# Kernel optimization log

Hardware: AMD Instinct MI355X
Metric: run time of the kernel (lower is better)

## Reference

```python
import jax, jax.numpy as jnp
import numpy as np

B, C, E_OLD, U = 8, 128, 48000, 8000
E_NEW = E_OLD + 3 * U  # unroll_target = 72000


def setup_inputs() -> dict:
    key = jax.random.key(0)
    kf, kw, kp = jax.random.split(key, 3)
    features = jax.random.normal(kf, (B, C, E_OLD), dtype=jnp.float32)
    weights = jax.random.uniform(kw, (B, U, 2, 3), dtype=jnp.float32)
    # Per-mesh permutation of the unrolled edge slots -> disjoint index groups
    perms = jax.vmap(lambda k: jax.random.permutation(k, E_NEW))(
        jax.random.split(kp, B)
    ).astype(jnp.int32)
    old_idx = perms[:, :E_OLD]                      # slots of relocated old edges
    left_idx = old_idx[:, :U]                       # source edges of unpool events
    right_idx = old_idx[:, U:2 * U]
    new_block = perms[:, E_OLD:]                    # 3U brand-new slots
    new_idx = new_block[:, :U]
    new_left_idx = new_block[:, U:2 * U]
    new_right_idx = new_block[:, 2 * U:3 * U]
    return {
        "features": features,
        "weights": weights,
        "old_idx": old_idx,
        "left_idx": left_idx,
        "right_idx": right_idx,
        "new_idx": new_idx,
        "new_left_idx": new_left_idx,
        "new_right_idx": new_right_idx,
    }


def _unpool_one(feat, w, old_i, l_i, r_i, n_i, nl_i, nr_i):
    # feat: [C, E_OLD], w: [U, 2, 3]
    nf = jnp.zeros((feat.shape[0], E_NEW), feat.dtype).at[:, old_i].set(feat)
    lf = nf[:, l_i]                                 # [C, U] left source features
    rf = nf[:, r_i]                                 # [C, U]
    lw, rw = w[:, 0, :], w[:, 1, :]                 # [U, 3] each
    nf = nf.at[:, l_i].set(lf * lw[:, 0])
    nf = nf.at[:, nl_i].set(lf * lw[:, 1])
    nf = nf.at[:, r_i].set(rf * rw[:, 0])
    nf = nf.at[:, nr_i].set(rf * rw[:, 1])
    nf = nf.at[:, n_i].set((lf * lw[:, 2] + rf * rw[:, 2]) * 0.5)
    return nf


def reference(features, weights, old_idx, left_idx, right_idx, new_idx,
              new_left_idx, new_right_idx):
    return jax.vmap(_unpool_one)(features, weights, old_idx, left_idx,
                                 right_idx, new_idx, new_left_idx,
                                 new_right_idx)  # [B, C, E_NEW]
```

## Files before the change

kernel.cpp:

```cpp
#include <hip/hip_runtime.h>


constexpr int B_     = 8;
constexpr int C_     = 128;
constexpr int E_OLD_ = 48000;
constexpr int U_     = 8000;
constexpr int E_NEW_ = E_OLD_ + 3 * U_;
constexpr int T_PER_B = U_ + (E_OLD_ - 2 * U_);

__device__ __forceinline__ int4 pack_map(int s0, int s1, float w0, float w1) {
    return make_int4(s0, s1, __float_as_int(w0), __float_as_int(w1));
}

__global__ __launch_bounds__(256)
void build_map_kernel(const float* __restrict__ w,
                      const int*   __restrict__ old_idx,
                      const int*   __restrict__ new_idx,
                      const int*   __restrict__ new_left,
                      const int*   __restrict__ new_right,
                      int4*        __restrict__ map) {
    const int b = blockIdx.y;
    const int t = blockIdx.x * blockDim.x + threadIdx.x;
    if (t >= T_PER_B) return;

    int4* mb = map + (size_t)b * E_NEW_;

    if (t < U_) {
        const int u   = t;
        const int jl  = old_idx [b * E_OLD_ + u];
        const int jr  = old_idx [b * E_OLD_ + U_ + u];
        const int jn  = new_idx [b * U_ + u];
        const int jnl = new_left [b * U_ + u];
        const int jnr = new_right[b * U_ + u];

        const float* wp = w + ((size_t)b * U_ + u) * 6;
        const float lw0 = wp[0], lw1 = wp[1], lw2 = wp[2];
        const float rw0 = wp[3], rw1 = wp[4], rw2 = wp[5];

        mb[jl]  = pack_map(u,       u,       lw0,        0.f);
        mb[jnl] = pack_map(u,       u,       lw1,        0.f);
        mb[jr]  = pack_map(U_ + u,  U_ + u,  rw0,        0.f);
        mb[jnr] = pack_map(U_ + u,  U_ + u,  rw1,        0.f);
        mb[jn]  = pack_map(u,       U_ + u,  0.5f * lw2, 0.5f * rw2);
    } else {
        const int e = t + U_;
        const int j = old_idx[b * E_OLD_ + e];
        mb[j] = pack_map(e, e, 1.0f, 0.f);
    }
}

constexpr int TE = 128;
constexpr int TC = 64;

__global__ __launch_bounds__(256)
void transpose_kernel(const float* __restrict__ feat,
                      float*       __restrict__ featT,
                      int b0) {
    __shared__ float tile[TE][TC + 1];
    const int bl = blockIdx.z;
    const int b  = b0 + bl;
    const int e0 = blockIdx.x * TE;
    const int c0 = blockIdx.y * TC;
    const int t  = threadIdx.x;

    {
        const int eo = (t & 31) * 4;
        const int co = t >> 5;
        const float* fb = feat + (size_t)b * C_ * E_OLD_ + e0 + eo;
        #pragma unroll
        for (int i = 0; i < 8; ++i) {
            const int c = i * 8 + co;
            const float4 v = *(const float4*)(fb + (size_t)(c0 + c) * E_OLD_);
            tile[eo + 0][c] = v.x;
            tile[eo + 1][c] = v.y;
            tile[eo + 2][c] = v.z;
            tile[eo + 3][c] = v.w;
        }
    }
    __syncthreads();

    {
        const int c4 = (t & 15) * 4;
        const int eb = t >> 4;
        float* ft = featT + (size_t)bl * E_OLD_ * C_
                          + (size_t)e0 * C_ + c0 + c4;
        #pragma unroll
        for (int i = 0; i < 8; ++i) {
            const int e = i * 16 + eb;
            float4 v;
            v.x = tile[e][c4 + 0];
            v.y = tile[e][c4 + 1];
            v.z = tile[e][c4 + 2];
            v.w = tile[e][c4 + 3];
            *(float4*)(ft + (size_t)e * C_) = v;
        }
    }
}

constexpr int JT = 64;
constexpr int TILES_PER_B = E_NEW_ / JT;

__global__ __launch_bounds__(256)
void gatherT_kernel(const float* __restrict__ featT,
                    const int4*  __restrict__ map,
                    float*       __restrict__ out,
                    int b0, int nb) {
    __shared__ float tile[JT][133];
    const int bl    = blockIdx.x % nb;
    const int b     = b0 + bl;
    const int chunk = blockIdx.x / nb;
    const int j0    = chunk * JT;
    const int t     = threadIdx.x;

    {
        const int j  = t >> 2;
        const int cq = t & 3;
        const int4 m = map[(size_t)b * E_NEW_ + j0 + j];
        const float w0 = __int_as_float(m.z);
        const float w1 = __int_as_float(m.w);

        const float* fTb = featT + (size_t)bl * E_OLD_ * C_;
        const float4* r0 = (const float4*)(fTb + (size_t)m.x * C_) + cq * 8;

        float4 acc[8];
        #pragma unroll
        for (int i = 0; i < 8; ++i) {
            const float4 f = r0[i];
            acc[i].x = w0 * f.x;
            acc[i].y = w0 * f.y;
            acc[i].z = w0 * f.z;
            acc[i].w = w0 * f.w;
        }
        if (w1 != 0.f) {
            const float4* r1 = (const float4*)(fTb + (size_t)m.y * C_) + cq * 8;
            #pragma unroll
            for (int i = 0; i < 8; ++i) {
                const float4 f = r1[i];
                acc[i].x += w1 * f.x;
                acc[i].y += w1 * f.y;
                acc[i].z += w1 * f.z;
                acc[i].w += w1 * f.w;
            }
        }
        float* trow = &tile[j][cq * 32];
        #pragma unroll
        for (int i = 0; i < 8; ++i) {
            trow[4 * i + 0] = acc[i].x;
            trow[4 * i + 1] = acc[i].y;
            trow[4 * i + 2] = acc[i].z;
            trow[4 * i + 3] = acc[i].w;
        }
    }
    __syncthreads();

    {
        const int jj = t & 63;
        const int cg = t >> 6;
        const float* tr = &tile[jj][cg * 32];
        float* ob = out + (size_t)b * C_ * E_NEW_
                        + (size_t)(cg * 32) * E_NEW_ + j0 + jj;
        #pragma unroll
        for (int k = 0; k < 32; ++k)
            __builtin_nontemporal_store(tr[k], ob + (size_t)k * E_NEW_);
    }
}

constexpr int K2_BLOCK     = 256;
constexpr int CHUNKS_PER_B = (E_NEW_ + K2_BLOCK - 1) / K2_BLOCK;

__global__ __launch_bounds__(K2_BLOCK)
void gather_kernel(const float* __restrict__ feat,
                   const int4*  __restrict__ map,
                   float*       __restrict__ out) {
    const int b     = blockIdx.x % B_;
    const int chunk = blockIdx.x / B_;
    const int j     = chunk * K2_BLOCK + threadIdx.x;
    if (j >= E_NEW_) return;

    const int4 m  = map[(size_t)b * E_NEW_ + j];
    const int  s0 = m.x;
    const int  s1 = m.y;
    const float w0 = __int_as_float(m.z);
    const float w1 = __int_as_float(m.w);

    const float* fb = feat + (size_t)b * C_ * E_OLD_;
    float*       ob = out  + (size_t)b * C_ * E_NEW_ + j;

    #pragma unroll 4
    for (int c = 0; c < C_; ++c) {
        const float f0 = fb[s0];
        const float f1 = fb[s1];
        *ob = w0 * f0 + w1 * f1;
        fb += E_OLD_;
        ob += E_NEW_;
    }
}

extern "C" void kernel_launch(void* const* d_in, const int* in_sizes, int n_in,
                              void* d_out, int out_size, void* d_ws, size_t ws_size,
                              hipStream_t stream) {
    const float* feat      = (const float*)d_in[0];
    const float* w         = (const float*)d_in[1];
    const int*   old_idx   = (const int*)  d_in[2];
    const int*   new_idx   = (const int*)  d_in[5];
    const int*   new_left  = (const int*)  d_in[6];
    const int*   new_right = (const int*)  d_in[7];
    float*       out       = (float*)d_out;

    int4* map = (int4*)d_ws;
    const size_t map_bytes = (size_t)B_ * E_NEW_ * sizeof(int4);
    const size_t featT_off = (map_bytes + 255) & ~(size_t)255;
    const size_t featT_one = (size_t)E_OLD_ * C_ * sizeof(float);
    const size_t featT_all = (size_t)B_ * featT_one;
    float* featT = (float*)((char*)d_ws + featT_off);

    {
        dim3 block(256);
        dim3 grid((T_PER_B + 255) / 256, B_);
        build_map_kernel<<<grid, block, 0, stream>>>(
            w, old_idx, new_idx, new_left, new_right, map);
    }

    if (ws_size >= featT_off + featT_all) {
        {
            dim3 block(256);
            dim3 grid(E_OLD_ / TE, C_ / TC, B_);
            transpose_kernel<<<grid, block, 0, stream>>>(feat, featT, 0);
        }
        {
            dim3 block(256);
            dim3 grid(TILES_PER_B * B_);
            gatherT_kernel<<<grid, block, 0, stream>>>(featT, map, out, 0, B_);
        }
    } else if (ws_size >= featT_off + featT_one) {
        for (int b = 0; b < B_; ++b) {
            dim3 tblock(256);
            dim3 tgrid(E_OLD_ / TE, C_ / TC, 1);
            transpose_kernel<<<tgrid, tblock, 0, stream>>>(feat, featT, b);
            dim3 gblock(256);
            dim3 ggrid(TILES_PER_B);
            gatherT_kernel<<<ggrid, gblock, 0, stream>>>(featT, map, out, b, 1);
        }
    } else {
        dim3 block(K2_BLOCK);
        dim3 grid(CHUNKS_PER_B * B_);
        gather_kernel<<<grid, block, 0, stream>>>(feat, map, out);
    }
}
```

Before: 558.8 us.

## Software-pipeline per-batch transpose and gather in fused step kernels

Replaces the separate build-map, all-batch transpose and all-batch gather launches with a sequence of combined step kernels. Step k transposes batch k and gathers batch k-1 in the same grid, and step 0 also builds the index map. The aim is to overlap transpose reads with gather writes and to keep each batch's transposed features hot in cache until they are gathered. In exchange it adds more launches, a pipeline tail, and blocks that exit early with no work. The device-side bodies are factored into shared inline helpers, and the fallback paths are preserved.

```diff
diff --git a/kernel.cpp b/kernel.cpp
--- a/kernel.cpp
+++ b/kernel.cpp
@@ -8,8 +8,187 @@
 constexpr int E_NEW_ = E_OLD_ + 3 * U_;
 constexpr int T_PER_B = U_ + (E_OLD_ - 2 * U_);
 
+constexpr int TE = 128;
+constexpr int TC = 64;
+constexpr int JT = 64;
+
+constexpr int T_BLOCKS    = (E_OLD_ / TE) * (C_ / TC);
+constexpr int G_BLOCKS    = E_NEW_ / JT;
+constexpr int BM_BLOCKS   = (B_ * T_PER_B + 255) / 256;
+
+constexpr int LDS_WORDS = 64 * 133;
+
 __device__ __forceinline__ int4 pack_map(int s0, int s1, float w0, float w1) {
     return make_int4(s0, s1, __float_as_int(w0), __float_as_int(w1));
+}
+
+
+__device__ __forceinline__ void build_body(
+    const float* __restrict__ w,
+    const int*   __restrict__ old_idx,
+    const int*   __restrict__ new_idx,
+    const int*   __restrict__ new_left,
+    const int*   __restrict__ new_right,
+    int4*        __restrict__ map,
+    int b, int t) {
+    int4* mb = map + (size_t)b * E_NEW_;
+
+    if (t < U_) {
+        const int u   = t;
+        const int jl  = old_idx [b * E_OLD_ + u];
+        const int jr  = old_idx [b * E_OLD_ + U_ + u];
+        const int jn  = new_idx [b * U_ + u];
+        const int jnl = new_left [b * U_ + u];
+        const int jnr = new_right[b * U_ + u];
+
+        const float* wp = w + ((size_t)b * U_ + u) * 6;
+        const float lw0 = wp[0], lw1 = wp[1], lw2 = wp[2];
+        const float rw0 = wp[3], rw1 = wp[4], rw2 = wp[5];
+
+        mb[jl]  = pack_map(u,       u,       lw0,        0.f);
+        mb[jnl] = pack_map(u,       u,       lw1,        0.f);
+        mb[jr]  = pack_map(U_ + u,  U_ + u,  rw0,        0.f);
+        mb[jnr] = pack_map(U_ + u,  U_ + u,  rw1,        0.f);
+        mb[jn]  = pack_map(u,       U_ + u,  0.5f * lw2, 0.5f * rw2);
+    } else {
+        const int e = t + U_;
+        const int j = old_idx[b * E_OLD_ + e];
+        mb[j] = pack_map(e, e, 1.0f, 0.f);
+    }
+}
+
+__device__ __forceinline__ void transpose_body(
+    const float* __restrict__ feat,
+    float*       __restrict__ featT,
+    int b, int bl, int tileIdx, int t,
+    float* __restrict__ tile ) {
+    const int e0 = (tileIdx >> 1) * TE;
+    const int c0 = (tileIdx & 1) * TC;
+
+    {
+        const int eo = (t & 31) * 4;
+        const int co = t >> 5;
+        const float* fb = feat + (size_t)b * C_ * E_OLD_ + e0 + eo;
+        #pragma unroll
+        for (int i = 0; i < 8; ++i) {
+            const int c = i * 8 + co;
+            const float4 v = *(const float4*)(fb + (size_t)(c0 + c) * E_OLD_);
+            tile[(eo + 0) * 65 + c] = v.x;
+            tile[(eo + 1) * 65 + c] = v.y;
+            tile[(eo + 2) * 65 + c] = v.z;
+            tile[(eo + 3) * 65 + c] = v.w;
+        }
+    }
+    __syncthreads();
+    {
+        const int c4 = (t & 15) * 4;
+        const int eb = t >> 4;
+        float* ft = featT + (size_t)bl * E_OLD_ * C_
+                          + (size_t)e0 * C_ + c0 + c4;
+        #pragma unroll
+        for (int i = 0; i < 8; ++i) {
+            const int e = i * 16 + eb;
+            float4 v;
+            v.x = tile[e * 65 + c4 + 0];
+            v.y = tile[e * 65 + c4 + 1];
+            v.z = tile[e * 65 + c4 + 2];
+            v.w = tile[e * 65 + c4 + 3];
+            *(float4*)(ft + (size_t)e * C_) = v;
+        }
+    }
+}
+
+__device__ __forceinline__ void gather_body(
+    const float* __restrict__ featT,
+    const int4*  __restrict__ map,
+    float*       __restrict__ out,
+    int b, int bl, int chunk, int t,
+    float* __restrict__ tile ) {
+    const int j0 = chunk * JT;
+
+    {
+        const int j  = t >> 2;
+        const int cq = t & 3;
+        const int4 m = map[(size_t)b * E_NEW_ + j0 + j];
+        const float w0 = __int_as_float(m.z);
+        const float w1 = __int_as_float(m.w);
+
+        const float* fTb = featT + (size_t)bl * E_OLD_ * C_;
+        const float4* r0 = (const float4*)(fTb + (size_t)m.x * C_) + cq * 8;
+
+        float4 acc[8];
+        #pragma unroll
+        for (int i = 0; i < 8; ++i) {
+            const float4 f = r0[i];
+            acc[i].x = w0 * f.x;
+            acc[i].y = w0 * f.y;
+            acc[i].z = w0 * f.z;
+            acc[i].w = w0 * f.w;
+        }
+        if (w1 != 0.f) {
+            const float4* r1 = (const float4*)(fTb + (size_t)m.y * C_) + cq * 8;
+            #pragma unroll
+            for (int i = 0; i < 8; ++i) {
+                const float4 f = r1[i];
+                acc[i].x += w1 * f.x;
+                acc[i].y += w1 * f.y;
+                acc[i].z += w1 * f.z;
+                acc[i].w += w1 * f.w;
+            }
+        }
+        float* trow = tile + j * 133 + cq * 32;
+        #pragma unroll
+        for (int i = 0; i < 8; ++i) {
+            trow[4 * i + 0] = acc[i].x;
+            trow[4 * i + 1] = acc[i].y;
+            trow[4 * i + 2] = acc[i].z;
+            trow[4 * i + 3] = acc[i].w;
+        }
+    }
+    __syncthreads();
+    {
+        const int jj = t & 63;
+        const int cg = t >> 6;
+        const float* tr = tile + jj * 133 + cg * 32;
+        float* ob = out + (size_t)b * C_ * E_NEW_
+                        + (size_t)(cg * 32) * E_NEW_ + j0 + jj;
+        #pragma unroll
+        for (int k = 0; k < 32; ++k)
+            __builtin_nontemporal_store(tr[k], ob + (size_t)k * E_NEW_);
+    }
+}
+
+__global__ __launch_bounds__(256)
+void pipe_step_kernel(const float* __restrict__ feat,
+                      float*       __restrict__ featT,
+                      const float* __restrict__ w,
+                      const int*   __restrict__ old_idx,
+                      const int*   __restrict__ new_idx,
+                      const int*   __restrict__ new_left,
+                      const int*   __restrict__ new_right,
+                      int4*        __restrict__ map,
+                      float*       __restrict__ out,
+                      int k) {
+    __shared__ float lds[LDS_WORDS];
+    int bid = blockIdx.x;
+    const int t = threadIdx.x;
+
+    if (bid < T_BLOCKS) {
+        if (k < B_)
+            transpose_body(feat, featT, k, k, bid, t, lds);
+        return;
+    }
+    bid -= T_BLOCKS;
+    if (bid < G_BLOCKS) {
+        if (k >= 1)
+            gather_body(featT, map, out, k - 1, k - 1, bid, t, lds);
+        return;
+    }
+    bid -= G_BLOCKS;
+    const int tg = bid * 256 + t;
+    if (tg < B_ * T_PER_B)
+        build_body(w, old_idx, new_idx, new_left, new_right, map,
+                   tg / T_PER_B, tg % T_PER_B);
 }
 
 __global__ __launch_bounds__(256)
@@ -22,147 +201,27 @@
     const int b = blockIdx.y;
     const int t = blockIdx.x * blockDim.x + threadIdx.x;
     if (t >= T_PER_B) return;
-
-    int4* mb = map + (size_t)b * E_NEW_;
-
-    if (t < U_) {
-        const int u   = t;
-        const int jl  = old_idx [b * E_OLD_ + u];
-        const int jr  = old_idx [b * E_OLD_ + U_ + u];
-        const int jn  = new_idx [b * U_ + u];
-        const int jnl = new_left [b * U_ + u];
-        const int jnr = new_right[b * U_ + u];
-
-        const float* wp = w + ((size_t)b * U_ + u) * 6;
-        const float lw0 = wp[0], lw1 = wp[1], lw2 = wp[2];
-        const float rw0 = wp[3], rw1 = wp[4], rw2 = wp[5];
-
-        mb[jl]  = pack_map(u,       u,       lw0,        0.f);
-        mb[jnl] = pack_map(u,       u,       lw1,        0.f);
-        mb[jr]  = pack_map(U_ + u,  U_ + u,  rw0,        0.f);
-        mb[jnr] = pack_map(U_ + u,  U_ + u,  rw1,        0.f);
-        mb[jn]  = pack_map(u,       U_ + u,  0.5f * lw2, 0.5f * rw2);
-    } else {
-        const int e = t + U_;
-        const int j = old_idx[b * E_OLD_ + e];
-        mb[j] = pack_map(e, e, 1.0f, 0.f);
-    }
-}
-
-constexpr int TE = 128;
-constexpr int TC = 64;
+    build_body(w, old_idx, new_idx, new_left, new_right, map, b, t);
+}
 
 __global__ __launch_bounds__(256)
 void transpose_kernel(const float* __restrict__ feat,
                       float*       __restrict__ featT,
                       int b0) {
-    __shared__ float tile[TE][TC + 1];
-    const int bl = blockIdx.z;
-    const int b  = b0 + bl;
-    const int e0 = blockIdx.x * TE;
-    const int c0 = blockIdx.y * TC;
-    const int t  = threadIdx.x;
-
-    {
-        const int eo = (t & 31) * 4;
-        const int co = t >> 5;
-        const float* fb = feat + (size_t)b * C_ * E_OLD_ + e0 + eo;
-        #pragma unroll
-        for (int i = 0; i < 8; ++i) {
-            const int c = i * 8 + co;
-            const float4 v = *(const float4*)(fb + (size_t)(c0 + c) * E_OLD_);
-            tile[eo + 0][c] = v.x;
-            tile[eo + 1][c] = v.y;
-            tile[eo + 2][c] = v.z;
-            tile[eo + 3][c] = v.w;
-        }
-    }
-    __syncthreads();
-
-    {
-        const int c4 = (t & 15) * 4;
-        const int eb = t >> 4;
-        float* ft = featT + (size_t)bl * E_OLD_ * C_
-                          + (size_t)e0 * C_ + c0 + c4;
-        #pragma unroll
-        for (int i = 0; i < 8; ++i) {
-            const int e = i * 16 + eb;
-            float4 v;
-            v.x = tile[e][c4 + 0];
-            v.y = tile[e][c4 + 1];
-            v.z = tile[e][c4 + 2];
-            v.w = tile[e][c4 + 3];
-            *(float4*)(ft + (size_t)e * C_) = v;
-        }
-    }
-}
-
-constexpr int JT = 64;
-constexpr int TILES_PER_B = E_NEW_ / JT;
+    __shared__ float lds[TE * (TC + 1)];
+    transpose_body(feat, featT, b0 + (int)blockIdx.z, (int)blockIdx.z,
+                   (int)blockIdx.x, (int)threadIdx.x, lds);
+}
 
 __global__ __launch_bounds__(256)
 void gatherT_kernel(const float* __restrict__ featT,
                     const int4*  __restrict__ map,
                     float*       __restrict__ out,
                     int b0, int nb) {
-    __shared__ float tile[JT][133];
+    __shared__ float lds[JT * 133];
     const int bl    = blockIdx.x % nb;
-    const int b     = b0 + bl;
     const int chunk = blockIdx.x / nb;
-    const int j0    = chunk * JT;
-    const int t     = threadIdx.x;
-
-    {
-        const int j  = t >> 2;
-        const int cq = t & 3;
-        const int4 m = map[(size_t)b * E_NEW_ + j0 + j];
-        const float w0 = __int_as_float(m.z);
-        const float w1 = __int_as_float(m.w);
-
-        const float* fTb = featT + (size_t)bl * E_OLD_ * C_;
-        const float4* r0 = (const float4*)(fTb + (size_t)m.x * C_) + cq * 8;
-
-        float4 acc[8];
-        #pragma unroll
-        for (int i = 0; i < 8; ++i) {
-            const float4 f = r0[i];
-            acc[i].x = w0 * f.x;
-            acc[i].y = w0 * f.y;
-            acc[i].z = w0 * f.z;
-            acc[i].w = w0 * f.w;
-        }
-        if (w1 != 0.f) {
-            const float4* r1 = (const float4*)(fTb + (size_t)m.y * C_) + cq * 8;
-            #pragma unroll
-            for (int i = 0; i < 8; ++i) {
-                const float4 f = r1[i];
-                acc[i].x += w1 * f.x;
-                acc[i].y += w1 * f.y;
-                acc[i].z += w1 * f.z;
-                acc[i].w += w1 * f.w;
-            }
-        }
-        float* trow = &tile[j][cq * 32];
-        #pragma unroll
-        for (int i = 0; i < 8; ++i) {
-            trow[4 * i + 0] = acc[i].x;
-            trow[4 * i + 1] = acc[i].y;
-            trow[4 * i + 2] = acc[i].z;
-            trow[4 * i + 3] = acc[i].w;
-        }
-    }
-    __syncthreads();
-
-    {
-        const int jj = t & 63;
-        const int cg = t >> 6;
-        const float* tr = &tile[jj][cg * 32];
-        float* ob = out + (size_t)b * C_ * E_NEW_
-                        + (size_t)(cg * 32) * E_NEW_ + j0 + jj;
-        #pragma unroll
-        for (int k = 0; k < 32; ++k)
-            __builtin_nontemporal_store(tr[k], ob + (size_t)k * E_NEW_);
-    }
+    gather_body(featT, map, out, b0 + bl, bl, chunk, (int)threadIdx.x, lds);
 }
 
 constexpr int K2_BLOCK     = 256;
@@ -178,8 +237,6 @@
     if (j >= E_NEW_) return;
 
     const int4 m  = map[(size_t)b * E_NEW_ + j];
-    const int  s0 = m.x;
-    const int  s1 = m.y;
     const float w0 = __int_as_float(m.z);
     const float w1 = __int_as_float(m.w);
 
@@ -188,8 +245,8 @@
 
     #pragma unroll 4
     for (int c = 0; c < C_; ++c) {
-        const float f0 = fb[s0];
-        const float f1 = fb[s1];
+        const float f0 = fb[m.x];
+        const float f1 = fb[m.y];
         *ob = w0 * f0 + w1 * f1;
         fb += E_OLD_;
         ob += E_NEW_;
@@ -214,34 +271,33 @@
     const size_t featT_all = (size_t)B_ * featT_one;
     float* featT = (float*)((char*)d_ws + featT_off);
 
-    {
-        dim3 block(256);
-        dim3 grid((T_PER_B + 255) / 256, B_);
-        build_map_kernel<<<grid, block, 0, stream>>>(
-            w, old_idx, new_idx, new_left, new_right, map);
-    }
-
     if (ws_size >= featT_off + featT_all) {
+        for (int k = 0; k <= B_; ++k) {
+            const int grid = T_BLOCKS + G_BLOCKS + (k == 0 ? BM_BLOCKS : 0);
+            pipe_step_kernel<<<dim3(grid), dim3(256), 0, stream>>>(
+                feat, featT, w, old_idx, new_idx, new_left, new_right,
+                map, out, k);
+        }
+    } else if (ws_size >= featT_off + featT_one) {
         {
             dim3 block(256);
-            dim3 grid(E_OLD_ / TE, C_ / TC, B_);
-            transpose_kernel<<<grid, block, 0, stream>>>(feat, featT, 0);
-        }
+            dim3 grid((T_PER_B + 255) / 256, B_);
+            build_map_kernel<<<grid, block, 0, stream>>>(
+                w, old_idx, new_idx, new_left, new_right, map);
+        }
+        for (int b = 0; b < B_; ++b) {
+            transpose_kernel<<<dim3(T_BLOCKS, 1, 1), dim3(256), 0, stream>>>(
+                feat, featT, b);
+            gatherT_kernel<<<dim3(G_BLOCKS), dim3(256), 0, stream>>>(
+                featT, map, out, b, 1);
+        }
+    } else {
         {
             dim3 block(256);
-            dim3 grid(TILES_PER_B * B_);
-            gatherT_kernel<<<grid, block, 0, stream>>>(featT, map, out, 0, B_);
-        }
-    } else if (ws_size >= featT_off + featT_one) {
-        for (int b = 0; b < B_; ++b) {
-            dim3 tblock(256);
-            dim3 tgrid(E_OLD_ / TE, C_ / TC, 1);
-            transpose_kernel<<<tgrid, tblock, 0, stream>>>(feat, featT, b);
-            dim3 gblock(256);
-            dim3 ggrid(TILES_PER_B);
-            gatherT_kernel<<<ggrid, gblock, 0, stream>>>(featT, map, out, b, 1);
-        }
-    } else {
+            dim3 grid((T_PER_B + 255) / 256, B_);
+            build_map_kernel<<<grid, block, 0, stream>>>(
+                w, old_idx, new_idx, new_left, new_right, map);
+        }
         dim3 block(K2_BLOCK);
         dim3 grid(CHUNKS_PER_B * B_);
         gather_kernel<<<grid, block, 0, stream>>>(feat, map, out);
```

New measurement: 526.3 us. 1.06x faster.
